# Optimization experiments

Hardware: AMD Instinct MI355X
Metric: run time of the kernel (lower is better)

## Reference

```python
import jax, jax.numpy as jnp
import numpy as np

H = 16  # num_heads

def setup_inputs() -> dict:
    key = jax.random.key(0)
    ks = jax.random.split(key, 5)
    B, L, D = 2, 2048, 1024
    x = jax.random.normal(ks[0], (B, L, D), dtype=jnp.float32)
    # causal mask: masked_fill where mask == 0
    attn_mask = jnp.tril(jnp.ones((L, L), dtype=jnp.int32))
    scale = 1.0 / np.sqrt(D)
    Wq = jax.random.normal(ks[1], (D, D), dtype=jnp.float32) * scale
    Wk = jax.random.normal(ks[2], (D, D), dtype=jnp.float32) * scale
    Wv = jax.random.normal(ks[3], (D, D), dtype=jnp.float32) * scale
    Wo = jax.random.normal(ks[4], (D, D), dtype=jnp.float32) * scale
    return {"x": x, "attn_mask": attn_mask, "Wq": Wq, "Wk": Wk, "Wv": Wv, "Wo": Wo}

def reference(x, attn_mask, Wq, Wk, Wv, Wo):
    B, L, D = x.shape
    dh = D // H
    # nn.Linear with no bias: y = x @ W^T
    q = (x @ Wq.T).reshape(B, L, H, dh)
    k = (x @ Wk.T).reshape(B, L, H, dh)
    v = (x @ Wv.T).reshape(B, L, H, dh)
    # scores: [B, H, L, L]
    scores = jnp.einsum('blhd,bmhd->bhlm', q, k) / jnp.sqrt(jnp.array(dh, x.dtype))
    scores = jnp.where(attn_mask == 0, -jnp.inf, scores)
    attn = jax.nn.softmax(scores, axis=-1)
    out = jnp.einsum('bhlm,bmhd->blhd', attn, v).reshape(B, L, D)
    return out @ Wo.T
```

## Files before the change

kernel.cpp:

```cpp
#include <hip/hip_runtime.h>
#include <math.h>

#define L_SEQ  2048
#define D_MODEL 1024
#define N_HEAD 16
#define D_HEAD 64
#define B_SIZE 2

typedef __attribute__((ext_vector_type(8))) short bf16x8;
typedef __attribute__((ext_vector_type(4))) float f32x4;
typedef unsigned short u16;
typedef unsigned int u32;

__device__ __forceinline__ f32x4 mfma16(bf16x8 a, bf16x8 b, f32x4 c) {
    return __builtin_amdgcn_mfma_f32_16x16x32_bf16(a, b, c, 0, 0, 0);
}

__device__ __forceinline__ u16 f2bf(float x) {
    u32 u = __builtin_bit_cast(u32, x);
    u32 r = (u + 0x7FFFu + ((u >> 16) & 1u)) >> 16;
    return (u16)r;
}
__device__ __forceinline__ u16 f2bf_t(float x) {
    return (u16)(__builtin_bit_cast(u32, x) >> 16);
}
__device__ __forceinline__ float bf2f(u16 h) {
    u32 u = ((u32)h) << 16;
    return __builtin_bit_cast(float, u);
}

__device__ __forceinline__ void gl2lds16(const void* g, void* l) {
    __builtin_amdgcn_global_load_lds(
        (__attribute__((address_space(1))) void*)(g),
        (__attribute__((address_space(3))) void*)(l), 16, 0, 0);
}

__global__ __launch_bounds__(256) void split_hl(const float* __restrict__ in,
                                                u16* __restrict__ out) {
    const int idx = blockIdx.x * 256 + threadIdx.x;
    const int c4 = idx << 2;
    const int r = c4 >> 10, c = c4 & 1023;
    float4 v = *(const float4*)(in + c4);
    u16 h0 = f2bf(v.x), h1 = f2bf(v.y), h2 = f2bf(v.z), h3 = f2bf(v.w);
    ushort4 hi = make_ushort4(h0, h1, h2, h3);
    ushort4 lo = make_ushort4(f2bf(v.x - bf2f(h0)), f2bf(v.y - bf2f(h1)),
                              f2bf(v.z - bf2f(h2)), f2bf(v.w - bf2f(h3)));
    *(ushort4*)(out + (size_t)r * 2048 + c) = hi;
    *(ushort4*)(out + (size_t)r * 2048 + 1024 + c) = lo;
}

__global__ __launch_bounds__(256) void split_w4(
    const float* __restrict__ w0, const float* __restrict__ w1,
    const float* __restrict__ w2, const float* __restrict__ w3,
    u16* __restrict__ outbase) {
    const float* in = (blockIdx.y == 0) ? w0 : (blockIdx.y == 1) ? w1
                      : (blockIdx.y == 2) ? w2 : w3;
    u16* out = outbase + (size_t)blockIdx.y * 2097152;
    const int idx = blockIdx.x * 256 + threadIdx.x;
    const int c4 = idx << 2;
    const int r = c4 >> 10, c = c4 & 1023;
    float4 v = *(const float4*)(in + c4);
    u16 h0 = f2bf(v.x), h1 = f2bf(v.y), h2 = f2bf(v.z), h3 = f2bf(v.w);
    ushort4 hi = make_ushort4(h0, h1, h2, h3);
    ushort4 lo = make_ushort4(f2bf(v.x - bf2f(h0)), f2bf(v.y - bf2f(h1)),
                              f2bf(v.z - bf2f(h2)), f2bf(v.w - bf2f(h3)));
    *(ushort4*)(out + (size_t)r * 2048 + c) = hi;
    *(ushort4*)(out + (size_t)r * 2048 + 1024 + c) = lo;
}

template <int MODE>
__global__ __launch_bounds__(256) void gemm_ks(
    const u16* __restrict__ A2, const u16* __restrict__ Wbase,
    float* __restrict__ Cout,
    u16* __restrict__ Qh, u16* __restrict__ Ql,
    u16* __restrict__ Kh, u16* __restrict__ Kl,
    u16* __restrict__ Vh, u16* __restrict__ Vl) {
    __shared__ __align__(16) u16 As[128 * 32];
    __shared__ __align__(16) u16 Ws[128 * 32];
    const int t = threadIdx.x, l = t & 63, wid = t >> 6;
    const int m0 = blockIdx.y << 7, n0 = blockIdx.x << 7;
    const int z = (MODE == 1) ? blockIdx.z : 0;
    const u16* W2 = Wbase + (size_t)z * (1024 * 2048);

    f32x4 acc[4][4];
#pragma unroll
    for (int i = 0; i < 4; ++i)
#pragma unroll
        for (int j = 0; j < 4; ++j) acc[i][j] = (f32x4){0.f, 0.f, 0.f, 0.f};

    int orow[2], ocs[2];
#pragma unroll
    for (int p = 0; p < 2; ++p) {
        int o = wid * 1024 + l * 16 + p * 4096;
        orow[p] = o >> 6;
        ocs[p] = ((o >> 4) & 3) ^ ((o >> 6) & 3);
    }
    const int wr = (wid >> 1) << 6, wc = (wid & 1) << 6;

    for (int k0 = 0; k0 < 3072; k0 += 32) {
        const int rg3 = k0 >> 10, kb = k0 & 1023;
        const int ka = (rg3 == 1 ? 1024 : 0) + kb;
        const int kw = (rg3 == 0 ? 1024 : 0) + kb;
        __syncthreads();
#pragma unroll
        for (int p = 0; p < 2; ++p) {
            gl2lds16(A2 + (size_t)(m0 + orow[p]) * 2048 + ka + ocs[p] * 8,
                     (u16*)As + (wid * 512 + p * 2048));
            gl2lds16(W2 + (size_t)(n0 + orow[p]) * 2048 + kw + ocs[p] * 8,
                     (u16*)Ws + (wid * 512 + p * 2048));
        }
        __syncthreads();
        bf16x8 af[4], bfr[4];
#pragma unroll
        for (int f = 0; f < 4; ++f) {
            int row = wr + (f << 4) + (l & 15);
            int ch = (l >> 4) ^ (row & 3);
            af[f] = *(const bf16x8*)&As[(row << 5) + (ch << 3)];
            int rown = wc + (f << 4) + (l & 15);
            int chn = (l >> 4) ^ (rown & 3);
            bfr[f] = *(const bf16x8*)&Ws[(rown << 5) + (chn << 3)];
        }
#pragma unroll
        for (int fm = 0; fm < 4; ++fm)
#pragma unroll
            for (int fn = 0; fn < 4; ++fn)
                acc[fm][fn] = mfma16(af[fm], bfr[fn], acc[fm][fn]);
    }

#pragma unroll
    for (int fm = 0; fm < 4; ++fm)
#pragma unroll
        for (int fn = 0; fn < 4; ++fn)
#pragma unroll
            for (int rg = 0; rg < 4; ++rg) {
                int gm = m0 + wr + (fm << 4) + ((l >> 4) << 2) + rg;
                int gn = n0 + wc + (fn << 4) + (l & 15);
                float v = acc[fm][fn][rg];
                if (MODE == 0) {
                    Cout[(size_t)gm * 1024 + gn] = v;
                } else {
                    if (z == 0) v *= 0.125f;
                    int b = gm >> 11, lq = gm & 2047, h = gn >> 6, d = gn & 63;
                    size_t oi = (((size_t)(b * 16 + h)) * 2048 + lq) * 64 + d;
                    u16 hi = f2bf(v);
                    u16 *ph, *pl;
                    if (z == 0)      { ph = Qh; pl = Ql; }
                    else if (z == 1) { ph = Kh; pl = Kl; }
                    else             { ph = Vh; pl = Vl; }
                    ph[oi] = hi;
                    if (z != 2) pl[oi] = f2bf(v - bf2f(hi));
                }
            }
}

__global__ __launch_bounds__(128) void vtrans(const u16* __restrict__ Vh,
                                              u16* __restrict__ Vth) {
    const int t = threadIdx.x;
    const int kt = (blockIdx.x << 1) + (t >> 6);
    const int h = blockIdx.y, b = blockIdx.z;
    const size_t base = ((size_t)(b * 16 + h)) * 131072;
    const int kv0 = kt << 6;
    const int st = t & 63;
    const int r0 = (st >> 3) << 3;
    const int c0 = (st & 7) << 3;
    ushort4 inv[8][2];
#pragma unroll
    for (int j = 0; j < 8; ++j) {
        const u16* p = Vh + base + (size_t)(kv0 + r0 + j) * 64 + c0;
        inv[j][0] = *(const ushort4*)p;
        inv[j][1] = *(const ushort4*)(p + 4);
    }
#pragma unroll
    for (int i = 0; i < 8; ++i) {
        u16 o[8];
#pragma unroll
        for (int j = 0; j < 8; ++j) {
            ushort4 vv = inv[j][i >> 2];
            const int ii = i & 3;
            o[j] = (ii == 0) ? vv.x : (ii == 1) ? vv.y : (ii == 2) ? vv.z : vv.w;
        }
        u16* q = Vth + base + (size_t)(c0 + i) * 2048 + kv0 + r0;
        *(ushort4*)q = make_ushort4(o[0], o[1], o[2], o[3]);
        *(ushort4*)(q + 4) = make_ushort4(o[4], o[5], o[6], o[7]);
    }
}

struct QTileState {
    bf16x8 qhf[2], qlf[2];
    f32x4 oacc[4];
    float mrow[4], lrow[4];
};

__device__ __forceinline__ void qstate_init(
    QTileState& st, const u16* Qh, const u16* Ql, size_t hb, int q0, int w, int l) {
    const int rowq = q0 + (w << 4) + (l & 15);
#pragma unroll
    for (int kc = 0; kc < 2; ++kc) {
        const size_t off = hb + (size_t)rowq * 64 + (((kc << 2) + (l >> 4)) << 3);
        st.qhf[kc] = *(const bf16x8*)(Qh + off);
        st.qlf[kc] = *(const bf16x8*)(Ql + off);
    }
#pragma unroll
    for (int i = 0; i < 4; ++i) {
        st.oacc[i] = (f32x4){0.f, 0.f, 0.f, 0.f};
        st.mrow[i] = -INFINITY;
        st.lrow[i] = 0.f;
    }
}

__device__ __forceinline__ void fa_compute(
    QTileState& st, const u16* bKh, const u16* bKl,
    const u16* bVh, int kv0, int q0, int w, int l, u16* Pw) {
    if (kv0 > q0 + (w << 4) + 15) return;

    f32x4 sacc[4];
#pragma unroll
    for (int nf = 0; nf < 4; ++nf) sacc[nf] = (f32x4){0.f, 0.f, 0.f, 0.f};
#pragma unroll
    for (int kc = 0; kc < 2; ++kc) {
        bf16x8 kh_[4], kl_[4];
#pragma unroll
        for (int nf = 0; nf < 4; ++nf) {
            const int row = (nf << 4) + (l & 15);
            const int ch = ((kc << 2) + (l >> 4)) ^ (row & 7);
            kh_[nf] = *(const bf16x8*)&bKh[(row << 6) + (ch << 3)];
            kl_[nf] = *(const bf16x8*)&bKl[(row << 6) + (ch << 3)];
        }
        __builtin_amdgcn_s_setprio(1);
#pragma unroll
        for (int nf = 0; nf < 4; ++nf) {
            sacc[nf] = mfma16(st.qhf[kc], kl_[nf], sacc[nf]);
            sacc[nf] = mfma16(st.qlf[kc], kh_[nf], sacc[nf]);
            sacc[nf] = mfma16(st.qhf[kc], kh_[nf], sacc[nf]);
        }
        __builtin_amdgcn_s_setprio(0);
    }

    const bool domask = (kv0 + 63) > (q0 + (w << 4));
    float pm[4] = {-INFINITY, -INFINITY, -INFINITY, -INFINITY};
    float sv[4][4];
#pragma unroll
    for (int nf = 0; nf < 4; ++nf)
#pragma unroll
        for (int rg = 0; rg < 4; ++rg) {
            float x = sacc[nf][rg];
            if (domask) {
                const int colg = kv0 + (nf << 4) + (l & 15);
                const int rowg = q0 + (w << 4) + ((l >> 4) << 2) + rg;
                if (colg > rowg) x = -INFINITY;
            }
            sv[nf][rg] = x;
            pm[rg] = fmaxf(pm[rg], x);
        }
#pragma unroll
    for (int rg = 0; rg < 4; ++rg) {
        float v = pm[rg];
        v = fmaxf(v, __shfl_xor(v, 1));
        v = fmaxf(v, __shfl_xor(v, 2));
        v = fmaxf(v, __shfl_xor(v, 4));
        v = fmaxf(v, __shfl_xor(v, 8));
        pm[rg] = v;
    }
    const float need = fmaxf(fmaxf(pm[0] - st.mrow[0], pm[1] - st.mrow[1]),
                             fmaxf(pm[2] - st.mrow[2], pm[3] - st.mrow[3]));
    if (__any(need > 8.0f)) {
#pragma unroll
        for (int rg = 0; rg < 4; ++rg) {
            const float mn = fmaxf(st.mrow[rg], pm[rg]);
            const float al = __expf(st.mrow[rg] - mn);
            st.mrow[rg] = mn;
            st.lrow[rg] *= al;
#pragma unroll
            for (int nf = 0; nf < 4; ++nf) st.oacc[nf][rg] *= al;
        }
    }
    float ps[4] = {0.f, 0.f, 0.f, 0.f};
    u16 pb[4][4];
#pragma unroll
    for (int nf = 0; nf < 4; ++nf)
#pragma unroll
        for (int rg = 0; rg < 4; ++rg) {
            const float p = __expf(sv[nf][rg] - st.mrow[rg]);
            ps[rg] += p;
            pb[nf][rg] = f2bf_t(p);
        }
#pragma unroll
    for (int rg = 0; rg < 4; ++rg) {
        float v = ps[rg];
        v += __shfl_xor(v, 1);
        v += __shfl_xor(v, 2);
        v += __shfl_xor(v, 4);
        v += __shfl_xor(v, 8);
        st.lrow[rg] += v;
    }

#pragma unroll
    for (int nf = 0; nf < 4; ++nf)
#pragma unroll
        for (int rg = 0; rg < 4; ++rg) {
            const int r = ((l >> 4) << 2) + rg;
            const int c = (nf << 4) + (l & 15);
            const int ch = (c >> 3) ^ (r & 7);
            Pw[(r << 6) + (ch << 3) + (c & 7)] = pb[nf][rg];
        }
#pragma unroll
    for (int kc = 0; kc < 2; ++kc) {
        const int r = l & 15;
        const int chp = ((kc << 2) + (l >> 4)) ^ (r & 7);
        const bf16x8 pa = *(const bf16x8*)&Pw[(r << 6) + (chp << 3)];
        bf16x8 vh_[4];
#pragma unroll
        for (int nf = 0; nf < 4; ++nf) {
            const int row = (nf << 4) + (l & 15);
            const int cv = ((kc << 2) + (l >> 4)) ^ (row & 7);
            vh_[nf] = *(const bf16x8*)&bVh[(row << 6) + (cv << 3)];
        }
        __builtin_amdgcn_s_setprio(1);
#pragma unroll
        for (int nf = 0; nf < 4; ++nf)
            st.oacc[nf] = mfma16(pa, vh_[nf], st.oacc[nf]);
        __builtin_amdgcn_s_setprio(0);
    }
}

__device__ __forceinline__ void fa_epilogue(
    QTileState& st, u16* A2, int g, int q0, int w, int l) {
    const int b = g >> 4, h = g & 15;
    float inv[4];
#pragma unroll
    for (int rg = 0; rg < 4; ++rg) inv[rg] = 1.0f / st.lrow[rg];
#pragma unroll
    for (int nf = 0; nf < 4; ++nf)
#pragma unroll
        for (int rg = 0; rg < 4; ++rg) {
            const int rowq = q0 + (w << 4) + ((l >> 4) << 2) + rg;
            const int m = (b << 11) + rowq;
            const int d = (nf << 4) + (l & 15);
            const float v = st.oacc[nf][rg] * inv[rg];
            const u16 hi = f2bf(v);
            const u16 lo = f2bf(v - bf2f(hi));
            const size_t rb = (size_t)m * 2048;
            A2[rb + h * 64 + d] = hi;
            A2[rb + 1024 + h * 64 + d] = lo;
        }
}

__global__ __launch_bounds__(512) void flash_mfma(
    const u16* __restrict__ Qh, const u16* __restrict__ Ql,
    const u16* __restrict__ Kh, const u16* __restrict__ Kl,
    const u16* __restrict__ Vth,
    u16* __restrict__ A2) {
    extern __shared__ __align__(16) u16 smem[];
    u16* const KhsA = smem;
    u16* const KlsA = smem + 4096;
    u16* const VhsA = smem + 8192;
    u16* const KhsB = smem + 12288;
    u16* const KlsB = smem + 16384;
    u16* const VhsB = smem + 20480;
    u16* const Ps   = smem + 24576;

    const int t = threadIdx.x, l = t & 63, w = t >> 6;
    const int id = blockIdx.x;
    const int nid = ((id & 7) << 5) + (id >> 3);
    const int g = nid >> 3;
    const int p = nid & 7;
    const int q0A = p << 7;
    const int q0B = (15 - p) << 7;
    const size_t hb = (size_t)g * 131072;

    QTileState stA, stB;
    qstate_init(stA, Qh, Ql, hb, q0A, w, l);
    qstate_init(stB, Qh, Ql, hb, q0B, w, l);

    const int row_s = t >> 3;
    const int cs_s = (t & 7) ^ (row_s & 7);

    auto stage = [&](u16* dKh, u16* dKl, u16* dVh, int kt_) {
        const int kv0s = kt_ << 6;
        const size_t koff = hb + (size_t)(kv0s + row_s) * 64 + cs_s * 8;
        gl2lds16(Kh + koff, dKh + t * 8);
        gl2lds16(Kl + koff, dKl + t * 8);
        const size_t voff = hb + (size_t)row_s * 2048 + kv0s + cs_s * 8;
        gl2lds16(Vth + voff, dVh + t * 8);
    };

    u16* const Pw = Ps + (w << 10);
    const int ntA = (p << 1) + 2;
    const int ntB = 32 - (p << 1);

    stage(KhsA, KlsA, VhsA, 0);
    __syncthreads();
    for (int kt = 0; kt < ntB; kt += 2) {
        stage(KhsB, KlsB, VhsB, kt + 1);
        fa_compute(stB, KhsA, KlsA, VhsA, kt << 6, q0B, w, l, Pw);
        if (kt < ntA)
            fa_compute(stA, KhsA, KlsA, VhsA, kt << 6, q0A, w, l, Pw);
        __syncthreads();
        if (kt + 2 < ntB) stage(KhsA, KlsA, VhsA, kt + 2);
        fa_compute(stB, KhsB, KlsB, VhsB, (kt + 1) << 6, q0B, w, l, Pw);
        if (kt + 1 < ntA)
            fa_compute(stA, KhsB, KlsB, VhsB, (kt + 1) << 6, q0A, w, l, Pw);
        __syncthreads();
    }

    fa_epilogue(stA, A2, g, q0A, w, l);
    fa_epilogue(stB, A2, g, q0B, w, l);
}

__global__ __launch_bounds__(256) void gemm_bt_f32(
    const float* __restrict__ A, const float* __restrict__ W,
    float* __restrict__ C, int M, int N, int K) {
    __shared__ float As[16][68];
    __shared__ float Bs[16][68];
    const int t = threadIdx.x;
    const int tx = t & 15, ty = t >> 4;
    const int m0 = blockIdx.y << 6, n0 = blockIdx.x << 6;
    const int lr = t >> 2, lc = (t & 3) << 2;
    const float* Ag = A + (size_t)(m0 + lr) * K + lc;
    const float* Wg = W + (size_t)(n0 + lr) * K + lc;
    float acc[4][4];
#pragma unroll
    for (int i = 0; i < 4; ++i)
#pragma unroll
        for (int j = 0; j < 4; ++j) acc[i][j] = 0.f;
    for (int k0 = 0; k0 < K; k0 += 16) {
        const float4 av = *(const float4*)(Ag + k0);
        const float4 wv = *(const float4*)(Wg + k0);
        __syncthreads();
        As[lc + 0][lr] = av.x; As[lc + 1][lr] = av.y;
        As[lc + 2][lr] = av.z; As[lc + 3][lr] = av.w;
        Bs[lc + 0][lr] = wv.x; Bs[lc + 1][lr] = wv.y;
        Bs[lc + 2][lr] = wv.z; Bs[lc + 3][lr] = wv.w;
        __syncthreads();
#pragma unroll
        for (int kk = 0; kk < 16; ++kk) {
            const float4 a = *(const float4*)&As[kk][ty << 2];
            const float4 b = *(const float4*)&Bs[kk][tx << 2];
            acc[0][0] += a.x * b.x; acc[0][1] += a.x * b.y; acc[0][2] += a.x * b.z; acc[0][3] += a.x * b.w;
            acc[1][0] += a.y * b.x; acc[1][1] += a.y * b.y; acc[1][2] += a.y * b.z; acc[1][3] += a.y * b.w;
            acc[2][0] += a.z * b.x; acc[2][1] += a.z * b.y; acc[2][2] += a.z * b.z; acc[2][3] += a.z * b.w;
            acc[3][0] += a.w * b.x; acc[3][1] += a.w * b.y; acc[3][2] += a.w * b.z; acc[3][3] += a.w * b.w;
        }
    }
#pragma unroll
    for (int i = 0; i < 4; ++i) {
        float4 o;
        o.x = acc[i][0]; o.y = acc[i][1]; o.z = acc[i][2]; o.w = acc[i][3];
        *(float4*)&C[(size_t)(m0 + (ty << 2) + i) * N + n0 + (tx << 2)] = o;
    }
}

#define SW(row, seg) ((((seg) ^ (((row) + ((row) >> 4)) & 15)) << 2))

__global__ __launch_bounds__(256) void flash_f32(
    const float* __restrict__ Q, const float* __restrict__ K,
    const float* __restrict__ V, float* __restrict__ O) {
    __shared__ float Qs[64 * 64];
    __shared__ float KPs[64 * 64];
    __shared__ float Vs[64 * 64];
    const int t = threadIdx.x;
    const int tx = t & 15, ty = t >> 4;
    const int qt = blockIdx.x, h = blockIdx.y, b = blockIdx.z;
    const int q0 = qt << 6;
    const size_t hbase = (size_t)b * L_SEQ * D_MODEL + (size_t)h * D_HEAD;
#pragma unroll
    for (int i = 0; i < 4; ++i) {
        const int idx = t + (i << 8);
        const int rr = idx >> 4, seg = idx & 15;
        const float4 qv = *(const float4*)&Q[hbase + (size_t)(q0 + rr) * D_MODEL + (seg << 2)];
        *(float4*)&Qs[rr * 64 + SW(rr, seg)] = qv;
    }
    float m[4], lr_[4], oacc[4][4];
#pragma unroll
    for (int i = 0; i < 4; ++i) {
        m[i] = -INFINITY; lr_[i] = 0.f;
#pragma unroll
        for (int j = 0; j < 4; ++j) oacc[i][j] = 0.f;
    }
    const int ntile = qt + 1;
    for (int kt = 0; kt < ntile; ++kt) {
        const int kv0 = kt << 6;
        __syncthreads();
#pragma unroll
        for (int i = 0; i < 4; ++i) {
            const int idx = t + (i << 8);
            const int rr = idx >> 4, seg = idx & 15;
            const float4 kv = *(const float4*)&K[hbase + (size_t)(kv0 + rr) * D_MODEL + (seg << 2)];
            const float4 vv = *(const float4*)&V[hbase + (size_t)(kv0 + rr) * D_MODEL + (seg << 2)];
            *(float4*)&KPs[rr * 64 + SW(rr, seg)] = kv;
            *(float4*)&Vs[rr * 64 + SW(rr, seg)] = vv;
        }
        __syncthreads();
        float s[4][4];
#pragma unroll
        for (int i = 0; i < 4; ++i)
#pragma unroll
            for (int j = 0; j < 4; ++j) s[i][j] = 0.f;
#pragma unroll
        for (int seg = 0; seg < 16; ++seg) {
            float4 qv[4], kv[4];
#pragma unroll
            for (int i = 0; i < 4; ++i) {
                const int R = (ty << 2) + i;
                qv[i] = *(const float4*)&Qs[R * 64 + SW(R, seg)];
            }
#pragma unroll
            for (int j = 0; j < 4; ++j) {
                const int Cc = (tx << 2) + j;
                kv[j] = *(const float4*)&KPs[Cc * 64 + SW(Cc, seg)];
            }
#pragma unroll
            for (int i = 0; i < 4; ++i)
#pragma unroll
                for (int j = 0; j < 4; ++j)
                    s[i][j] += qv[i].x * kv[j].x + qv[i].y * kv[j].y +
                               qv[i].z * kv[j].z + qv[i].w * kv[j].w;
        }
        const bool diag = (kt == qt);
        float tm[4];
#pragma unroll
        for (int i = 0; i < 4; ++i) {
            tm[i] = -INFINITY;
#pragma unroll
            for (int j = 0; j < 4; ++j) {
                float sval = s[i][j] * 0.125f;
                if (diag) {
                    const int Cg = kv0 + (tx << 2) + j;
                    const int Rg = q0 + (ty << 2) + i;
                    if (Cg > Rg) sval = -INFINITY;
                }
                s[i][j] = sval;
                tm[i] = fmaxf(tm[i], sval);
            }
            tm[i] = fmaxf(tm[i], __shfl_xor(tm[i], 1));
            tm[i] = fmaxf(tm[i], __shfl_xor(tm[i], 2));
            tm[i] = fmaxf(tm[i], __shfl_xor(tm[i], 4));
            tm[i] = fmaxf(tm[i], __shfl_xor(tm[i], 8));
        }
        float p[4][4];
#pragma unroll
        for (int i = 0; i < 4; ++i) {
            const float mn = fmaxf(m[i], tm[i]);
            const float alpha = __expf(m[i] - mn);
            m[i] = mn;
            float psum = 0.f;
#pragma unroll
            for (int j = 0; j < 4; ++j) {
                p[i][j] = __expf(s[i][j] - mn);
                psum += p[i][j];
            }
            psum += __shfl_xor(psum, 1);
            psum += __shfl_xor(psum, 2);
            psum += __shfl_xor(psum, 4);
            psum += __shfl_xor(psum, 8);
            lr_[i] = lr_[i] * alpha + psum;
#pragma unroll
            for (int j = 0; j < 4; ++j) oacc[i][j] *= alpha;
        }
        __syncthreads();
#pragma unroll
        for (int i = 0; i < 4; ++i) {
            const int R = (ty << 2) + i;
            float4 pv;
            pv.x = p[i][0]; pv.y = p[i][1]; pv.z = p[i][2]; pv.w = p[i][3];
            *(float4*)&KPs[R * 64 + SW(R, tx)] = pv;
        }
        __syncthreads();
#pragma unroll
        for (int cs = 0; cs < 16; ++cs) {
            float pc[4][4];
            float4 vr[4];
#pragma unroll
            for (int i = 0; i < 4; ++i) {
                const int R = (ty << 2) + i;
                const float4 pr = *(const float4*)&KPs[R * 64 + SW(R, cs)];
                pc[i][0] = pr.x; pc[i][1] = pr.y; pc[i][2] = pr.z; pc[i][3] = pr.w;
            }
#pragma unroll
            for (int cc = 0; cc < 4; ++cc) {
                const int Cr = (cs << 2) + cc;
                vr[cc] = *(const float4*)&Vs[Cr * 64 + SW(Cr, tx)];
            }
#pragma unroll
            for (int i = 0; i < 4; ++i)
#pragma unroll
                for (int cc = 0; cc < 4; ++cc) {
                    oacc[i][0] += pc[i][cc] * vr[cc].x;
                    oacc[i][1] += pc[i][cc] * vr[cc].y;
                    oacc[i][2] += pc[i][cc] * vr[cc].z;
                    oacc[i][3] += pc[i][cc] * vr[cc].w;
                }
        }
    }
#pragma unroll
    for (int i = 0; i < 4; ++i) {
        const int R = (ty << 2) + i;
        const float invl = 1.0f / lr_[i];
        float4 o;
        o.x = oacc[i][0] * invl; o.y = oacc[i][1] * invl;
        o.z = oacc[i][2] * invl; o.w = oacc[i][3] * invl;
        *(float4*)&O[hbase + (size_t)(q0 + R) * D_MODEL + (tx << 2)] = o;
    }
}

extern "C" void kernel_launch(void* const* d_in, const int* in_sizes, int n_in,
                              void* d_out, int out_size, void* d_ws, size_t ws_size,
                              hipStream_t stream) {
    const float* x  = (const float*)d_in[0];
    const float* Wq = (const float*)d_in[2];
    const float* Wk = (const float*)d_in[3];
    const float* Wv = (const float*)d_in[4];
    const float* Wo = (const float*)d_in[5];
    float* out = (float*)d_out;

    if (ws_size >= 83886080ull) {
        char* ws = (char*)d_ws;
        u16* x2  = (u16*)(ws);
        u16* Wq2 = (u16*)(ws + 16777216);
        u16* Wo2 = (u16*)(ws + 29360128);
        u16* Qh  = (u16*)(ws + 33554432);
        u16* Ql  = (u16*)(ws + 41943040);
        u16* Kh  = (u16*)(ws + 50331648);
        u16* Kl  = (u16*)(ws + 58720256);
        u16* Vth = (u16*)(ws + 67108864);
        u16* Vh  = (u16*)d_out;
        u16* Vl  = (u16*)d_out + 4194304;

        hipFuncSetAttribute((const void*)flash_mfma,
                            hipFuncAttributeMaxDynamicSharedMemorySize, 65536);

        split_hl<<<4096, 256, 0, stream>>>(x, x2);
        split_w4<<<dim3(1024, 4), 256, 0, stream>>>(Wq, Wk, Wv, Wo, Wq2);
        gemm_ks<1><<<dim3(8, 32, 3), 256, 0, stream>>>(x2, Wq2, nullptr,
                                                       Qh, Ql, Kh, Kl, Vh, Vl);
        vtrans<<<dim3(16, 16, 2), 128, 0, stream>>>(Vh, Vth);
        flash_mfma<<<256, 512, 65536, stream>>>(Qh, Ql, Kh, Kl, Vth, x2);
        gemm_ks<0><<<dim3(8, 32, 1), 256, 0, stream>>>(x2, Wo2, out,
                                                       nullptr, nullptr, nullptr,
                                                       nullptr, nullptr, nullptr);
    } else {
        const int M = B_SIZE * L_SEQ, N = D_MODEL, Kd = D_MODEL;
        float* Qw = (float*)d_ws;
        float* Kw = Qw + (size_t)M * D_MODEL;
        float* Vw = Kw + (size_t)M * D_MODEL;
        float* Aw = Vw + (size_t)M * D_MODEL;
        dim3 gg(N / 64, M / 64);
        gemm_bt_f32<<<gg, 256, 0, stream>>>(x, Wq, Qw, M, N, Kd);
        gemm_bt_f32<<<gg, 256, 0, stream>>>(x, Wk, Kw, M, N, Kd);
        gemm_bt_f32<<<gg, 256, 0, stream>>>(x, Wv, Vw, M, N, Kd);
        flash_f32<<<dim3(L_SEQ / 64, N_HEAD, B_SIZE), 256, 0, stream>>>(Qw, Kw, Vw, Aw);
        gemm_bt_f32<<<gg, 256, 0, stream>>>(Aw, Wo, out, M, N, Kd);
    }
}
```

Baseline: 249.3 us.

## Replace QKV projection GEMM with fused 256x256-tile pipelined MFMA kernel

```diff
diff --git a/kernel.cpp b/kernel.cpp
--- a/kernel.cpp
+++ b/kernel.cpp
@@ -68,19 +68,178 @@
     *(ushort4*)(out + (size_t)r * 2048 + 1024 + c) = lo;
 }
 
+__device__ __forceinline__ int kaOf(int x) {
+    return (((x >> 4) == 1) ? 1024 : 0) + ((x << 6) & 1023);
+}
+__device__ __forceinline__ int kwOf(int x) {
+    return (((x >> 4) == 0) ? 1024 : 0) + ((x << 6) & 1023);
+}
+
+#define SBAR()  do { __builtin_amdgcn_sched_barrier(0); \
+                     __builtin_amdgcn_s_barrier(); \
+                     __builtin_amdgcn_sched_barrier(0); } while (0)
+
+__global__ __launch_bounds__(512) void gemm256_qkv(
+    const u16* __restrict__ A2, const u16* __restrict__ Wall,
+    u16* __restrict__ Qh, u16* __restrict__ Ql,
+    u16* __restrict__ Kh, u16* __restrict__ Kl,
+    u16* __restrict__ Vh) {
+    extern __shared__ __align__(16) u16 smem[];
+
+    const int t = threadIdx.x, l = t & 63, wid = t >> 6;
+    const int id = blockIdx.x;
+    const int wg = (id & 7) * 24 + (id >> 3);
+    const int mt = wg / 12, ntile = wg % 12;
+    const int m0 = mt << 8, n0 = ntile << 8;
+
+    const int wrH = wid >> 2;
+    const int wc = (wid & 3) << 6;
+    const int bHalf = (wid & 3) >> 1;
+    const int brB = (wid & 1) << 6;
+
+    f32x4 acc[8][4];
+#pragma unroll
+    for (int i = 0; i < 8; ++i)
+#pragma unroll
+        for (int j = 0; j < 4; ++j) acc[i][j] = (f32x4){0.f, 0.f, 0.f, 0.f};
+
+    const int sr = t >> 3, sc = t & 7;
+
+    auto stageA = [&](int x, int half) {
+        const int koff = kaOf(x);
+        u16* dst = smem + ((x & 1) * 32768) + half * 8192;
+        const u16* srcb = A2 + (size_t)(m0 + half * 128) * 2048 + koff;
+#pragma unroll
+        for (int p = 0; p < 2; ++p) {
+            const int r = sr + p * 64;
+            const int ck = sc ^ (r & 7);
+            gl2lds16(srcb + (size_t)r * 2048 + ck * 8, dst + (t + p * 512) * 8);
+        }
+    };
+    auto stageB = [&](int x, int half) {
+        const int koff = kwOf(x);
+        u16* dst = smem + 16384 + ((x & 1) * 32768) + half * 8192;
+        const u16* srcb = Wall + (size_t)(n0 + half * 128) * 2048 + koff;
+#pragma unroll
+        for (int p = 0; p < 2; ++p) {
+            const int r = sr + p * 64;
+            const int ck = sc ^ (r & 7);
+            gl2lds16(srcb + (size_t)r * 2048 + ck * 8, dst + (t + p * 512) * 8);
+        }
+    };
+    auto dsA = [&](int s, int mh, int kc, bf16x8 af[4]) {
+        const u16* Ab = smem + s * 32768 + wrH * 8192;
+#pragma unroll
+        for (int f = 0; f < 4; ++f) {
+            const int r = mh * 64 + f * 16 + (l & 15);
+            const int c8 = kc * 4 + (l >> 4);
+            af[f] = *(const bf16x8*)&Ab[r * 64 + ((c8 ^ (r & 7)) << 3)];
+        }
+    };
+    auto dsB = [&](int s, int kc, bf16x8 bfr[4]) {
+        const u16* Bb = smem + 16384 + s * 32768 + bHalf * 8192;
+#pragma unroll
+        for (int f = 0; f < 4; ++f) {
+            const int r = brB + f * 16 + (l & 15);
+            const int c8 = kc * 4 + (l >> 4);
+            bfr[f] = *(const bf16x8*)&Bb[r * 64 + ((c8 ^ (r & 7)) << 3)];
+        }
+    };
+
+    stageB(0, 0); stageB(0, 1); stageA(0, 0); stageA(0, 1);
+    stageB(1, 0); stageB(1, 1);
+    __builtin_amdgcn_sched_barrier(0);
+    asm volatile("s_waitcnt vmcnt(4)" ::: "memory");
+    __builtin_amdgcn_s_barrier();
+    __builtin_amdgcn_sched_barrier(0);
+
+    const int NT = 48;
+    bf16x8 breg0[4], breg1[4], af[4];
+    for (int tt = 0; tt < NT; ++tt) {
+        const int s = tt & 1;
+        dsA(s, 0, 0, af); dsB(s, 0, breg0);
+        if (tt + 1 < NT) stageA(tt + 1, 0);
+        SBAR();
+        __builtin_amdgcn_s_setprio(1);
+#pragma unroll
+        for (int f = 0; f < 4; ++f)
+#pragma unroll
+            for (int fn = 0; fn < 4; ++fn)
+                acc[f][fn] = mfma16(af[f], breg0[fn], acc[f][fn]);
+        __builtin_amdgcn_s_setprio(0);
+        SBAR();
+        dsA(s, 0, 1, af); dsB(s, 1, breg1);
+        if (tt + 1 < NT) stageA(tt + 1, 1);
+        SBAR();
+        __builtin_amdgcn_s_setprio(1);
+#pragma unroll
+        for (int f = 0; f < 4; ++f)
+#pragma unroll
+            for (int fn = 0; fn < 4; ++fn)
+                acc[f][fn] = mfma16(af[f], breg1[fn], acc[f][fn]);
+        __builtin_amdgcn_s_setprio(0);
+        SBAR();
+        dsA(s, 1, 0, af);
+        if (tt + 2 < NT) stageB(tt + 2, 0);
+        SBAR();
+        __builtin_amdgcn_s_setprio(1);
+#pragma unroll
+        for (int f = 0; f < 4; ++f)
+#pragma unroll
+            for (int fn = 0; fn < 4; ++fn)
+                acc[4 + f][fn] = mfma16(af[f], breg0[fn], acc[4 + f][fn]);
+        __builtin_amdgcn_s_setprio(0);
+        SBAR();
+        dsA(s, 1, 1, af);
+        if (tt + 2 < NT) stageB(tt + 2, 1);
+        SBAR();
+        __builtin_amdgcn_s_setprio(1);
+#pragma unroll
+        for (int f = 0; f < 4; ++f)
+#pragma unroll
+            for (int fn = 0; fn < 4; ++fn)
+                acc[4 + f][fn] = mfma16(af[f], breg1[fn], acc[4 + f][fn]);
+        __builtin_amdgcn_s_setprio(0);
+        __builtin_amdgcn_sched_barrier(0);
+        if (tt + 2 < NT) {
+            asm volatile("s_waitcnt vmcnt(4)" ::: "memory");
+        } else if (tt + 1 < NT) {
+            asm volatile("s_waitcnt vmcnt(0)" ::: "memory");
+        }
+        __builtin_amdgcn_s_barrier();
+        __builtin_amdgcn_sched_barrier(0);
+    }
+
+#pragma unroll
+    for (int fm = 0; fm < 8; ++fm)
+#pragma unroll
+        for (int fn = 0; fn < 4; ++fn)
+#pragma unroll
+            for (int rg = 0; rg < 4; ++rg) {
+                const int gm = m0 + wrH * 128 + fm * 16 + ((l >> 4) << 2) + rg;
+                const int gn = n0 + wc + fn * 16 + (l & 15);
+                const int z = gn >> 10, col = gn & 1023;
+                float v = acc[fm][fn][rg];
+                if (z == 0) v *= 0.125f;
+                const int b = gm >> 11, lq = gm & 2047;
+                const int h = col >> 6, d = col & 63;
+                const size_t oi = (((size_t)(b * 16 + h)) * 2048 + lq) * 64 + d;
+                const u16 hi = f2bf(v);
+                if (z == 0) { Qh[oi] = hi; Ql[oi] = f2bf(v - bf2f(hi)); }
+                else if (z == 1) { Kh[oi] = hi; Kl[oi] = f2bf(v - bf2f(hi)); }
+                else { Vh[oi] = hi; }
+            }
+}
+
 template <int MODE>
 __global__ __launch_bounds__(256) void gemm_ks(
     const u16* __restrict__ A2, const u16* __restrict__ Wbase,
-    float* __restrict__ Cout,
-    u16* __restrict__ Qh, u16* __restrict__ Ql,
-    u16* __restrict__ Kh, u16* __restrict__ Kl,
-    u16* __restrict__ Vh, u16* __restrict__ Vl) {
+    float* __restrict__ Cout) {
     __shared__ __align__(16) u16 As[128 * 32];
     __shared__ __align__(16) u16 Ws[128 * 32];
     const int t = threadIdx.x, l = t & 63, wid = t >> 6;
     const int m0 = blockIdx.y << 7, n0 = blockIdx.x << 7;
-    const int z = (MODE == 1) ? blockIdx.z : 0;
-    const u16* W2 = Wbase + (size_t)z * (1024 * 2048);
+    const u16* W2 = Wbase;
 
     f32x4 acc[4][4];
 #pragma unroll
@@ -135,21 +294,7 @@
             for (int rg = 0; rg < 4; ++rg) {
                 int gm = m0 + wr + (fm << 4) + ((l >> 4) << 2) + rg;
                 int gn = n0 + wc + (fn << 4) + (l & 15);
-                float v = acc[fm][fn][rg];
-                if (MODE == 0) {
-                    Cout[(size_t)gm * 1024 + gn] = v;
-                } else {
-                    if (z == 0) v *= 0.125f;
-                    int b = gm >> 11, lq = gm & 2047, h = gn >> 6, d = gn & 63;
-                    size_t oi = (((size_t)(b * 16 + h)) * 2048 + lq) * 64 + d;
-                    u16 hi = f2bf(v);
-                    u16 *ph, *pl;
-                    if (z == 0)      { ph = Qh; pl = Ql; }
-                    else if (z == 1) { ph = Kh; pl = Kl; }
-                    else             { ph = Vh; pl = Vl; }
-                    ph[oi] = hi;
-                    if (z != 2) pl[oi] = f2bf(v - bf2f(hi));
-                }
+                Cout[(size_t)gm * 1024 + gn] = acc[fm][fn][rg];
             }
 }
 
@@ -624,20 +769,18 @@
         u16* Kl  = (u16*)(ws + 58720256);
         u16* Vth = (u16*)(ws + 67108864);
         u16* Vh  = (u16*)d_out;
-        u16* Vl  = (u16*)d_out + 4194304;
 
         hipFuncSetAttribute((const void*)flash_mfma,
                             hipFuncAttributeMaxDynamicSharedMemorySize, 65536);
+        hipFuncSetAttribute((const void*)gemm256_qkv,
+                            hipFuncAttributeMaxDynamicSharedMemorySize, 131072);
 
         split_hl<<<4096, 256, 0, stream>>>(x, x2);
         split_w4<<<dim3(1024, 4), 256, 0, stream>>>(Wq, Wk, Wv, Wo, Wq2);
-        gemm_ks<1><<<dim3(8, 32, 3), 256, 0, stream>>>(x2, Wq2, nullptr,
-                                                       Qh, Ql, Kh, Kl, Vh, Vl);
+        gemm256_qkv<<<192, 512, 131072, stream>>>(x2, Wq2, Qh, Ql, Kh, Kl, Vh);
         vtrans<<<dim3(16, 16, 2), 128, 0, stream>>>(Vh, Vth);
         flash_mfma<<<256, 512, 65536, stream>>>(Qh, Ql, Kh, Kl, Vth, x2);
-        gemm_ks<0><<<dim3(8, 32, 1), 256, 0, stream>>>(x2, Wo2, out,
-                                                       nullptr, nullptr, nullptr,
-                                                       nullptr, nullptr, nullptr);
+        gemm_ks<0><<<dim3(8, 32), 256, 0, stream>>>(x2, Wo2, out);
     } else {
         const int M = B_SIZE * L_SEQ, N = D_MODEL, Kd = D_MODEL;
         float* Qw = (float*)d_ws;
```

Result: no change. 250.8 us (+0.6%).
